# Kernel optimization log

Measured on AMD Instinct MI355X. Metric: run time of the kernel, lower is better.

## Reference

```python
import jax, jax.numpy as jnp
import numpy as np


def setup_inputs() -> dict:
    key = jax.random.key(0)
    k1, k2, k3 = jax.random.split(key, 3)
    bsz, seqlen = 1024, 200
    vocab, d = 100000, 512
    xs = jax.random.randint(k1, (bsz, seqlen), 0, vocab, dtype=jnp.int64)
    lt_weight = jax.random.normal(k2, (vocab, d), dtype=jnp.float32)
    # freqs[i] = 1/(1+log(1+freq)) in the original -> positive weights in (0,1]
    freqs = jax.random.uniform(k3, (vocab,), dtype=jnp.float32, minval=0.05, maxval=1.0)
    return {"xs": xs, "lt_weight": lt_weight, "freqs": freqs}


def reference(xs, lt_weight, freqs):
    # embedding lookup: [bsz, len, d]
    xs_emb = lt_weight[xs]
    # vectorized replacement of the per-element python double loop:
    # x_scale[j, i] = freqs[xs[j, i]]  -> [bsz, len]
    x_scale = freqs[xs]
    # normalize by Frobenius norm of the whole [bsz, len] matrix (torch .norm())
    x_scale = x_scale / jnp.linalg.norm(x_scale)
    # weighted pooling: xs_emb^T @ x_scale -> [bsz, d]
    return jnp.einsum("bld,bl->bd", xs_emb, x_scale)
```

## Files before the change

### kernel.cpp

```cpp
#include <hip/hip_runtime.h>

#define SEQ 200
#define SEQ_PAD 256
#define DIM 512

__global__ __launch_bounds__(256) void ssq_kernel(const int* __restrict__ xs,
                                                  const float* __restrict__ freqs,
                                                  double* __restrict__ ssq,
                                                  int n) {
    double acc = 0.0;
    for (int i = blockIdx.x * blockDim.x + threadIdx.x; i < n;
         i += gridDim.x * blockDim.x) {
        float f = freqs[xs[i]];
        acc += (double)f * (double)f;
    }
    for (int off = 32; off > 0; off >>= 1)
        acc += __shfl_down(acc, off, 64);
    __shared__ double s_w[4];
    int lane = threadIdx.x & 63;
    int wave = threadIdx.x >> 6;
    if (lane == 0) s_w[wave] = acc;
    __syncthreads();
    if (threadIdx.x == 0) {
        double t = s_w[0] + s_w[1] + s_w[2] + s_w[3];
        atomicAdd(ssq, t);
    }
}

__global__ __launch_bounds__(512) void pool_kernel(const int* __restrict__ xs,
                                                   const float* __restrict__ W,
                                                   const float* __restrict__ freqs,
                                                   const double* __restrict__ ssq,
                                                   float* __restrict__ out) {
    __shared__ unsigned s_key[SEQ_PAD];
    __shared__ float    s_scl[SEQ];
    __shared__ float    s_part[3][DIM];

    const int b   = blockIdx.x;
    const int tid = threadIdx.x;

    const float inv_norm = (float)(1.0 / sqrt(ssq[0]));

    for (int l = tid; l < SEQ_PAD; l += 512) {
        if (l < SEQ) {
            int idx  = xs[b * SEQ + l];
            s_key[l] = ((unsigned)idx << 8) | (unsigned)l;
            s_scl[l] = freqs[idx] * inv_norm;
        } else {
            s_key[l] = 0xFFFFFFFFu;
        }
    }

    for (unsigned k = 2; k <= SEQ_PAD; k <<= 1) {
        for (unsigned j = k >> 1; j > 0; j >>= 1) {
            __syncthreads();
            if (tid < SEQ_PAD) {
                unsigned i = (unsigned)tid, ixj = i ^ j;
                if (ixj > i) {
                    unsigned a = s_key[i], c = s_key[ixj];
                    bool up = ((i & k) == 0);
                    if ((a > c) == up) { s_key[i] = c; s_key[ixj] = a; }
                }
            }
        }
    }
    __syncthreads();

    const int group   = tid >> 7;
    const int lane128 = tid & 127;
    const int col4    = lane128 * 4;

    float4 acc = make_float4(0.f, 0.f, 0.f, 0.f);

    #pragma unroll 4
    for (int l = group; l < SEQ; l += 4) {
        const unsigned key = s_key[l];
        const int   idx    = (int)(key >> 8);
        const float s      = s_scl[key & 255u];
        const float4 w     = *reinterpret_cast<const float4*>(
            W + (size_t)idx * DIM + col4);
        acc.x += s * w.x;
        acc.y += s * w.y;
        acc.z += s * w.z;
        acc.w += s * w.w;
    }

    if (group > 0)
        *reinterpret_cast<float4*>(&s_part[group - 1][col4]) = acc;
    __syncthreads();

    if (group == 0) {
        for (int g = 0; g < 3; ++g) {
            const float4 p = *reinterpret_cast<const float4*>(&s_part[g][col4]);
            acc.x += p.x; acc.y += p.y; acc.z += p.z; acc.w += p.w;
        }
        *reinterpret_cast<float4*>(out + (size_t)b * DIM + col4) = acc;
    }
}

extern "C" void kernel_launch(void* const* d_in, const int* in_sizes, int n_in,
                              void* d_out, int out_size, void* d_ws, size_t ws_size,
                              hipStream_t stream) {
    const int*   xs    = (const int*)d_in[0];
    const float* W     = (const float*)d_in[1];
    const float* freqs = (const float*)d_in[2];
    float* out = (float*)d_out;
    double* ssq = (double*)d_ws;

    const int n   = in_sizes[0];
    const int bsz = n / SEQ;

    hipMemsetAsync(d_ws, 0, sizeof(double), stream);
    ssq_kernel<<<400, 256, 0, stream>>>(xs, freqs, ssq, n);
    pool_kernel<<<bsz, 512, 0, stream>>>(xs, W, freqs, ssq, out);
}
```

Baseline: 81.22 us.

## Phase pooled gathers by vocab range with block barriers to align L2 locality

```diff
diff --git a/kernel.cpp b/kernel.cpp
--- a/kernel.cpp
+++ b/kernel.cpp
@@ -3,6 +3,7 @@
 #define SEQ 200
 #define SEQ_PAD 256
 #define DIM 512
+#define NPHASE 16
 
 __global__ __launch_bounds__(256) void ssq_kernel(const int* __restrict__ xs,
                                                   const float* __restrict__ freqs,
@@ -31,9 +32,11 @@
                                                    const float* __restrict__ W,
                                                    const float* __restrict__ freqs,
                                                    const double* __restrict__ ssq,
-                                                   float* __restrict__ out) {
+                                                   float* __restrict__ out,
+                                                   int vocab) {
     __shared__ unsigned s_key[SEQ_PAD];
     __shared__ float    s_scl[SEQ];
+    __shared__ int      s_ph[NPHASE + 1];
     __shared__ float    s_part[3][DIM];
 
     const int b   = blockIdx.x;
@@ -66,23 +69,39 @@
     }
     __syncthreads();
 
+    if (tid <= NPHASE) {
+        unsigned bound = (unsigned)(((unsigned long long)vocab * (unsigned)tid)
+                                    / NPHASE) << 8;
+        int lo = 0, hi = SEQ_PAD;
+        while (lo < hi) {
+            int mid = (lo + hi) >> 1;
+            if (s_key[mid] < bound) lo = mid + 1; else hi = mid;
+        }
+        s_ph[tid] = lo;
+    }
+    __syncthreads();
+
     const int group   = tid >> 7;
     const int lane128 = tid & 127;
     const int col4    = lane128 * 4;
 
     float4 acc = make_float4(0.f, 0.f, 0.f, 0.f);
 
-    #pragma unroll 4
-    for (int l = group; l < SEQ; l += 4) {
-        const unsigned key = s_key[l];
-        const int   idx    = (int)(key >> 8);
-        const float s      = s_scl[key & 255u];
-        const float4 w     = *reinterpret_cast<const float4*>(
-            W + (size_t)idx * DIM + col4);
-        acc.x += s * w.x;
-        acc.y += s * w.y;
-        acc.z += s * w.z;
-        acc.w += s * w.w;
+    for (int p = 0; p < NPHASE; ++p) {
+        const int beg = s_ph[p];
+        const int end = s_ph[p + 1];
+        for (int l = beg + group; l < end; l += 4) {
+            const unsigned key = s_key[l];
+            const int   idx    = (int)(key >> 8);
+            const float s      = s_scl[key & 255u];
+            const float4 w     = *reinterpret_cast<const float4*>(
+                W + (size_t)idx * DIM + col4);
+            acc.x += s * w.x;
+            acc.y += s * w.y;
+            acc.z += s * w.z;
+            acc.w += s * w.w;
+        }
+        __syncthreads();
     }
 
     if (group > 0)
@@ -91,8 +110,8 @@
 
     if (group == 0) {
         for (int g = 0; g < 3; ++g) {
-            const float4 p = *reinterpret_cast<const float4*>(&s_part[g][col4]);
-            acc.x += p.x; acc.y += p.y; acc.z += p.z; acc.w += p.w;
+            const float4 p4 = *reinterpret_cast<const float4*>(&s_part[g][col4]);
+            acc.x += p4.x; acc.y += p4.y; acc.z += p4.z; acc.w += p4.w;
         }
         *reinterpret_cast<float4*>(out + (size_t)b * DIM + col4) = acc;
     }
@@ -107,10 +126,11 @@
     float* out = (float*)d_out;
     double* ssq = (double*)d_ws;
 
-    const int n   = in_sizes[0];
-    const int bsz = n / SEQ;
+    const int n     = in_sizes[0];
+    const int bsz   = n / SEQ;
+    const int vocab = in_sizes[2];
 
     hipMemsetAsync(d_ws, 0, sizeof(double), stream);
     ssq_kernel<<<400, 256, 0, stream>>>(xs, freqs, ssq, n);
-    pool_kernel<<<bsz, 512, 0, stream>>>(xs, W, freqs, ssq, out);
+    pool_kernel<<<bsz, 512, 0, stream>>>(xs, W, freqs, ssq, out, vocab);
 }
```

After: 74.92 us. 7.7% less time.
